# Performance work log

Hardware: AMD Instinct MI355X
Metric: run time of the kernel (lower is better)

The kernel has to match this reference:

```python
import jax, jax.numpy as jnp
import numpy as np

B, T, D, H = 4, 1024, 1024, 16
HD = D // H
EPS = 1e-5


def setup_inputs() -> dict:
    key = jax.random.key(0)
    ks = jax.random.split(key, 8)
    input_tensor = jax.random.normal(ks[0], (B, T, D), dtype=jnp.float32)
    # contiguous valid prefixes (realistic padding mask); True = valid
    lengths = jax.random.randint(ks[1], (B,), T // 2, T + 1)
    sequence_mask = jnp.arange(T)[None, :] < lengths[:, None]
    # online attention mask: causal (True = position allowed)
    attn_mask = jnp.tril(jnp.ones((T, T), dtype=bool))
    scale = 1.0 / np.sqrt(D)
    in_proj_w = jax.random.normal(ks[2], (3 * D, D), dtype=jnp.float32) * scale
    in_proj_b = jnp.zeros((3 * D,), dtype=jnp.float32)
    out_w = jax.random.normal(ks[3], (D, D), dtype=jnp.float32) * scale
    out_b = jnp.zeros((D,), dtype=jnp.float32)
    ln_gamma = jnp.ones((D,), dtype=jnp.float32)
    ln_beta = jnp.zeros((D,), dtype=jnp.float32)
    return {
        "input_tensor": input_tensor,
        "ln_gamma": ln_gamma,
        "ln_beta": ln_beta,
        "in_proj_w": in_proj_w,
        "in_proj_b": in_proj_b,
        "out_w": out_w,
        "out_b": out_b,
        "sequence_mask": sequence_mask,
        "attn_mask": attn_mask,
    }


def reference(input_tensor, ln_gamma, ln_beta, in_proj_w, in_proj_b, out_w, out_b,
              sequence_mask, attn_mask):
    # LayerNorm over last dim
    mu = jnp.mean(input_tensor, axis=-1, keepdims=True)
    var = jnp.mean(jnp.square(input_tensor - mu), axis=-1, keepdims=True)
    x = (input_tensor - mu) * jax.lax.rsqrt(var + EPS) * ln_gamma + ln_beta

    # shared QKV projection (torch MHA packed in_proj)
    qkv = x @ in_proj_w.T + in_proj_b  # [B,T,3D]
    q, k, v = jnp.split(qkv, 3, axis=-1)
    q = q.reshape(B, T, H, HD) * (1.0 / np.sqrt(HD))
    k = k.reshape(B, T, H, HD)
    v = v.reshape(B, T, H, HD)

    scores = jnp.einsum("bqhd,bkhd->bhqk", q, k)  # [B,H,T,T], shared

    keypad = sequence_mask[:, None, None, :]          # True = valid key
    online_ok = keypad & attn_mask[None, None, :, :]  # padding + attn mask
    neg_inf = jnp.float32(-jnp.inf)

    def attend(ok_mask):
        p = jax.nn.softmax(jnp.where(ok_mask, scores, neg_inf), axis=-1)
        o = jnp.einsum("bhqk,bkhd->bqhd", p, v).reshape(B, T, D)
        return o @ out_w.T + out_b

    out_online = attend(online_ok)   # key_padding + attn_mask
    out_offline = attend(keypad)     # key_padding only (full context)
    # training path: cat on dim 0 then view(2, B, T, D)
    return jnp.stack((out_online, out_offline), axis=0)
```

## Files before the change

kernel.cpp:

```cpp
#include <hip/hip_runtime.h>

#define B_ 4
#define T_ 1024
#define D_ 1024
#define H_ 16
#define HD_ 64

typedef unsigned short u16;
typedef __bf16 bf16x8 __attribute__((ext_vector_type(8)));
typedef float f32x4 __attribute__((ext_vector_type(4)));
typedef unsigned short u16x4 __attribute__((ext_vector_type(4)));

__device__ inline u16 f2b(float f) {
    union { float f; unsigned u; } v; v.f = f;
    unsigned r = v.u + 0x7fffu + ((v.u >> 16) & 1u);
    return (u16)(r >> 16);
}

__device__ inline f32x4 mfma16(bf16x8 a, bf16x8 b, f32x4 c) {
    return __builtin_amdgcn_mfma_f32_16x16x32_bf16(a, b, c, 0, 0, 0);
}

__global__ __launch_bounds__(256) void len_kernel(const unsigned char* __restrict__ m,
                                                  int* __restrict__ lens) {
    const int t = threadIdx.x;
    const int b = blockIdx.x;
    const int esz4 = (m[1] == 0);
    int c = 0;
    for (int i = t; i < T_; i += 256) {
        bool v = esz4 ? (((const int*)m)[b * T_ + i] != 0) : (m[b * T_ + i] != 0);
        c += v ? 1 : 0;
    }
#pragma unroll
    for (int off = 1; off < 64; off <<= 1) c += __shfl_xor(c, off);
    __shared__ int red[4];
    if ((t & 63) == 0) red[t >> 6] = c;
    __syncthreads();
    if (t == 0) lens[b] = red[0] + red[1] + red[2] + red[3];
}

__global__ __launch_bounds__(256) void cvt_bf16(const float* __restrict__ in,
                                                u16* __restrict__ out, int n4) {
    int i = blockIdx.x * 256 + threadIdx.x;
    int stride = gridDim.x * 256;
    for (; i < n4; i += stride) {
        float4 v = ((const float4*)in)[i];
        u16x4 o = { f2b(v.x), f2b(v.y), f2b(v.z), f2b(v.w) };
        ((u16x4*)out)[i] = o;
    }
}

__global__ __launch_bounds__(256) void ln_kernel(const float* __restrict__ x,
                                                 const float* __restrict__ g,
                                                 const float* __restrict__ be,
                                                 u16* __restrict__ y) {
    __shared__ float red[8];
    const int row = blockIdx.x;
    const int tid = threadIdx.x;
    const float* xr = x + (size_t)row * D_;
    float4 v = ((const float4*)xr)[tid];
    float s  = v.x + v.y + v.z + v.w;
    float ss = v.x*v.x + v.y*v.y + v.z*v.z + v.w*v.w;
#pragma unroll
    for (int off = 1; off < 64; off <<= 1) {
        s  += __shfl_xor(s, off);
        ss += __shfl_xor(ss, off);
    }
    const int w = tid >> 6;
    if ((tid & 63) == 0) { red[w*2] = s; red[w*2+1] = ss; }
    __syncthreads();
    s  = red[0] + red[2] + red[4] + red[6];
    ss = red[1] + red[3] + red[5] + red[7];
    const float mu = s * (1.f/1024.f);
    const float rs = rsqrtf(ss*(1.f/1024.f) - mu*mu + 1e-5f);
    float4 gv = ((const float4*)g)[tid];
    float4 bv = ((const float4*)be)[tid];
    u16x4 o = { f2b((v.x-mu)*rs*gv.x + bv.x),
                f2b((v.y-mu)*rs*gv.y + bv.y),
                f2b((v.z-mu)*rs*gv.z + bv.z),
                f2b((v.w-mu)*rs*gv.w + bv.w) };
    ((u16x4*)(y + (size_t)row * D_))[tid] = o;
}

template <int EPI>
__global__ __launch_bounds__(512) void gemm_bt(
    const u16* __restrict__ A, const u16* __restrict__ Bw,
    const float* __restrict__ bias, float* __restrict__ Cf,
    u16* __restrict__ Qb, u16* __restrict__ Kb, u16* __restrict__ Vt,
    int M, int N, int K, int MB) {
    __shared__ u16 As[2][256 * 64];
    __shared__ u16 Bs[2][256 * 64];
    const int tid = threadIdx.x;
    const int w = tid >> 6, l = tid & 63;
    const int l15 = l & 15, lg = l >> 4;
    const int wr = w >> 2, wc = w & 3;

    const int nwg = gridDim.x;
    const int q8 = nwg >> 3, r8 = nwg & 7;
    const int xcd = blockIdx.x & 7, pos = blockIdx.x >> 3;
    const int swz = (xcd < r8 ? xcd * (q8 + 1) : r8 * (q8 + 1) + (xcd - r8) * q8) + pos;
    const int m0 = (swz % MB) * 256;
    const int n0 = (swz / MB) * 256;

    const int srow = l >> 3;
    const int scg  = (l & 7) ^ srow;
    const int swa  = l15 & 7;

    f32x4 acc[8][4];
#pragma unroll
    for (int m = 0; m < 8; m++)
#pragma unroll
        for (int n = 0; n < 4; n++) acc[m][n] = (f32x4){0.f, 0.f, 0.f, 0.f};

    const int KS = K >> 6;

    auto stage = [&](int buf, int ks) {
        const int k0 = ks * 64;
#pragma unroll
        for (int it = 0; it < 4; ++it) {
            const int c = w * 4 + it;
            const int row = c * 8 + srow;
            const u16* ga = A  + (size_t)(m0 + row) * K + (k0 + scg * 8);
            const u16* gb = Bw + (size_t)(n0 + row) * K + (k0 + scg * 8);
            __builtin_amdgcn_global_load_lds(
                (const __attribute__((address_space(1))) unsigned int*)ga,
                (__attribute__((address_space(3))) unsigned int*)(&As[buf][c * 512]), 16, 0, 0);
            __builtin_amdgcn_global_load_lds(
                (const __attribute__((address_space(1))) unsigned int*)gb,
                (__attribute__((address_space(3))) unsigned int*)(&Bs[buf][c * 512]), 16, 0, 0);
        }
    };

    stage(0, 0);

    int buf = 0;
    for (int ks = 0; ks < KS; ++ks) {
        if (ks + 1 < KS) {
            stage(buf ^ 1, ks + 1);
            asm volatile("s_waitcnt vmcnt(8)" ::: "memory");
        } else {
            asm volatile("s_waitcnt vmcnt(0)" ::: "memory");
        }
        __builtin_amdgcn_sched_barrier(0);
        __builtin_amdgcn_s_barrier();
        __builtin_amdgcn_sched_barrier(0);
#pragma unroll
        for (int h = 0; h < 2; ++h) {
            bf16x8 bfr[4];
#pragma unroll
            for (int n = 0; n < 4; n++)
                bfr[n] = *(const bf16x8*)&Bs[buf][(wc*64 + n*16 + l15) * 64 + ((h*4 + lg) ^ swa) * 8];
#pragma unroll
            for (int m = 0; m < 8; m++) {
                bf16x8 af = *(const bf16x8*)&As[buf][(wr*128 + m*16 + l15) * 64 + ((h*4 + lg) ^ swa) * 8];
#pragma unroll
                for (int n = 0; n < 4; n++)
                    acc[m][n] = mfma16(af, bfr[n], acc[m][n]);
            }
        }
        __builtin_amdgcn_sched_barrier(0);
        __builtin_amdgcn_s_barrier();
        __builtin_amdgcn_sched_barrier(0);
        buf ^= 1;
    }

#pragma unroll
    for (int m = 0; m < 8; m++) {
#pragma unroll
        for (int n = 0; n < 4; n++) {
            const int col = n0 + wc*64 + n*16 + l15;
            const float bv = bias[col];
            if constexpr (EPI == 0) {
#pragma unroll
                for (int r = 0; r < 4; r++) {
                    const int row = m0 + wr*128 + m*16 + lg*4 + r;
                    Cf[(size_t)row * N + col] = acc[m][n][r] + bv;
                }
            } else {
                const int which = col >> 10;
                const int d = col & 1023;
                const int h = d >> 6, hd = d & 63;
#pragma unroll
                for (int r = 0; r < 4; r++) {
                    const int row = m0 + wr*128 + m*16 + lg*4 + r;
                    const int bb = row >> 10, t = row & 1023;
                    const float v = acc[m][n][r] + bv;
                    const size_t bh = (size_t)bb * H_ + h;
                    if (which == 0)      Qb[(bh * T_ + t) * HD_ + hd] = f2b(v * 0.125f);
                    else if (which == 1) Kb[(bh * T_ + t) * HD_ + hd] = f2b(v);
                    else                 Vt[(bh * HD_ + hd) * T_ + t] = f2b(v);
                }
            }
        }
    }
}

__global__ __launch_bounds__(256) void attn_kernel(
    const u16* __restrict__ Qb, const u16* __restrict__ Kb,
    const u16* __restrict__ Vt, const int* __restrict__ lens,
    u16* __restrict__ Ob) {
    __shared__ u16 Ks[2][64 * 64];
    __shared__ u16 Vs[2][64 * 64];
    __shared__ char Pl[4][2048];
    const int qt  = blockIdx.x;
    const int bh  = blockIdx.y;
    const int b = bh >> 4, h = bh & 15;
    const int tid = threadIdx.x, w = tid >> 6, l = tid & 63;
    const int l15 = l & 15, lg = l >> 4;
    const int len = lens[b];

    const u16* Qh = Qb + (size_t)bh * (T_ * HD_);
    const u16* Kh = Kb + (size_t)bh * (T_ * HD_);
    const u16* Vh = Vt + (size_t)bh * (HD_ * T_);

    const int q0 = qt * 64 + w * 16;
    const int qrow = q0 + l15;

    const bf16x8 qf0 = *(const bf16x8*)(Qh + (size_t)qrow * HD_ + lg * 8);
    const bf16x8 qf1 = *(const bf16x8*)(Qh + (size_t)qrow * HD_ + 32 + lg * 8);

    f32x4 acc0[4], acc1[4];
#pragma unroll
    for (int n = 0; n < 4; n++) {
        acc0[n] = (f32x4){0.f, 0.f, 0.f, 0.f};
        acc1[n] = (f32x4){0.f, 0.f, 0.f, 0.f};
    }
    float l0p = 0.f, l1p = 0.f;

    const int ntk = (len + 63) >> 6;

    char* Pw = &Pl[w][0];
    const int swz = (l15 & 7) << 4;
    const int rsw = l15 & 7;

    const int srow = l >> 3;
    const int scg  = (l & 7) ^ srow;

    const float C1 = 1.44269504f, C0 = -28.8539008f;

    auto stage = [&](int buf, int kt) {
        const int k0 = kt * 64;
#pragma unroll
        for (int c = 0; c < 2; ++c) {
            const int row = (w*2 + c)*8 + srow;
            const u16* gk = Kh + (size_t)(k0 + row) * HD_ + scg*8;
            const u16* gv = Vh + (size_t)row * T_ + k0 + scg*8;
            __builtin_amdgcn_global_load_lds(
                (const __attribute__((address_space(1))) unsigned int*)gk,
                (__attribute__((address_space(3))) unsigned int*)(&Ks[buf][(w*2+c)*512]), 16, 0, 0);
            __builtin_amdgcn_global_load_lds(
                (const __attribute__((address_space(1))) unsigned int*)gv,
                (__attribute__((address_space(3))) unsigned int*)(&Vs[buf][(w*2+c)*512]), 16, 0, 0);
        }
    };

    stage(0, 0);
    __syncthreads();

    int buf = 0;
    for (int kt = 0; kt < ntk; ++kt) {
        if (kt + 1 < ntk) stage(buf ^ 1, kt + 1);
        const int k0 = kt * 64;
        const u16* Kt = &Ks[buf][0];
        const u16* Vl = &Vs[buf][0];

        f32x4 s[4];
#pragma unroll
        for (int n = 0; n < 4; n++) {
            const u16* kr = Kt + (n*16 + l15) * 64;
            bf16x8 kf0 = *(const bf16x8*)&kr[((0 + lg) ^ rsw) * 8];
            bf16x8 kf1 = *(const bf16x8*)&kr[((4 + lg) ^ rsw) * 8];
            f32x4 z = (f32x4){0.f, 0.f, 0.f, 0.f};
            z = mfma16(kf0, qf0, z);
            z = mfma16(kf1, qf1, z);
            s[n] = z;
        }
        bf16x8 vf[4][2];
#pragma unroll
        for (int n = 0; n < 4; n++) {
            const u16* vr = Vl + (n*16 + l15) * 64;
            vf[n][0] = *(const bf16x8*)&vr[((0 + lg) ^ rsw) * 8];
            vf[n][1] = *(const bf16x8*)&vr[((4 + lg) ^ rsw) * 8];
        }
        float pn = 0.f;
#pragma unroll
        for (int n = 0; n < 4; n++) {
            const int kb = k0 + n*16 + lg*4;
#pragma unroll
            for (int r = 0; r < 4; r++) {
                const float e = (kb + r < len) ? exp2f(s[n][r]*C1 + C0) : 0.f;
                s[n][r] = e;
                pn += e;
            }
        }
        const bool diag = (kt == qt);
        if (diag) {
            l0p = l1p;
#pragma unroll
            for (int n = 0; n < 4; n++) acc0[n] = acc1[n];
        }
        l1p += pn;
#pragma unroll
        for (int n = 0; n < 4; n++) {
            u16x4 pk = { f2b(s[n][0]), f2b(s[n][1]), f2b(s[n][2]), f2b(s[n][3]) };
            *(u16x4*)(Pw + ((l15*128 + n*32 + lg*8) ^ swz)) = pk;
        }
#pragma unroll
        for (int kk = 0; kk < 2; ++kk) {
            bf16x8 pa = *(const bf16x8*)(Pw + ((l15*128 + kk*64 + lg*16) ^ swz));
#pragma unroll
            for (int n = 0; n < 4; n++)
                acc1[n] = mfma16(vf[n][kk], pa, acc1[n]);
        }
        if (diag) {
            float pn0 = 0.f;
#pragma unroll
            for (int n = 0; n < 4; n++) {
                const int kb = k0 + n*16 + lg*4;
#pragma unroll
                for (int r = 0; r < 4; r++) {
                    const float e = (kb + r <= qrow) ? s[n][r] : 0.f;
                    s[n][r] = e;
                    pn0 += e;
                }
            }
            l0p += pn0;
#pragma unroll
            for (int n = 0; n < 4; n++) {
                u16x4 pk = { f2b(s[n][0]), f2b(s[n][1]), f2b(s[n][2]), f2b(s[n][3]) };
                *(u16x4*)(Pw + ((l15*128 + n*32 + lg*8) ^ swz)) = pk;
            }
#pragma unroll
            for (int kk = 0; kk < 2; ++kk) {
                bf16x8 pa = *(const bf16x8*)(Pw + ((l15*128 + kk*64 + lg*16) ^ swz));
#pragma unroll
                for (int n = 0; n < 4; n++)
                    acc0[n] = mfma16(vf[n][kk], pa, acc0[n]);
            }
        }
        __syncthreads();
        buf ^= 1;
    }

    if (qt >= ntk) {
        l0p = l1p;
#pragma unroll
        for (int n = 0; n < 4; n++) acc0[n] = acc1[n];
    }

    float l0 = l0p + __shfl_xor(l0p, 16);
    l0 += __shfl_xor(l0, 32);
    float l1 = l1p + __shfl_xor(l1p, 16);
    l1 += __shfl_xor(l1, 32);

    const float inv0 = 1.f / l0;
    const float inv1 = 1.f / l1;
    u16* O0 = Ob + ((size_t)b * T_ + qrow) * D_ + h * HD_;
    u16* O1 = O0 + (size_t)B_ * T_ * D_;
#pragma unroll
    for (int n = 0; n < 4; n++) {
        u16x4 o0 = { f2b(acc0[n][0] * inv0), f2b(acc0[n][1] * inv0),
                     f2b(acc0[n][2] * inv0), f2b(acc0[n][3] * inv0) };
        u16x4 o1 = { f2b(acc1[n][0] * inv1), f2b(acc1[n][1] * inv1),
                     f2b(acc1[n][2] * inv1), f2b(acc1[n][3] * inv1) };
        *(u16x4*)(O0 + n*16 + lg*4) = o0;
        *(u16x4*)(O1 + n*16 + lg*4) = o1;
    }
}

extern "C" void kernel_launch(void* const* d_in, const int* in_sizes, int n_in,
                              void* d_out, int out_size, void* d_ws, size_t ws_size,
                              hipStream_t stream) {
    const float* x_in   = (const float*)d_in[0];
    const float* gamma  = (const float*)d_in[1];
    const float* beta   = (const float*)d_in[2];
    const float* wqkv_f = (const float*)d_in[3];
    const float* bqkv   = (const float*)d_in[4];
    const float* wout_f = (const float*)d_in[5];
    const float* bout   = (const float*)d_in[6];
    const unsigned char* smask = (const unsigned char*)d_in[7];
    float* out = (float*)d_out;

    char* ws = (char*)d_ws;
    u16* xb   = (u16*)(ws);
    u16* wqkv = (u16*)(ws + ((size_t)8  << 20));
    u16* wo   = (u16*)(ws + ((size_t)14 << 20));
    u16* Qb   = (u16*)(ws + ((size_t)16 << 20));
    u16* Kb   = (u16*)(ws + ((size_t)24 << 20));
    u16* Vt   = (u16*)(ws + ((size_t)32 << 20));
    u16* Ob   = (u16*)(ws + ((size_t)40 << 20));
    int* lens = (int*)(ws + ((size_t)56 << 20));

    len_kernel<<<dim3(B_), dim3(256), 0, stream>>>(smask, lens);
    cvt_bf16<<<dim3(1024), dim3(256), 0, stream>>>(wqkv_f, wqkv, (3 * D_ * D_) / 4);
    cvt_bf16<<<dim3(512),  dim3(256), 0, stream>>>(wout_f, wo, (D_ * D_) / 4);
    ln_kernel<<<dim3(B_ * T_), dim3(256), 0, stream>>>(x_in, gamma, beta, xb);
    gemm_bt<1><<<dim3(192), dim3(512), 0, stream>>>(
        xb, wqkv, bqkv, nullptr, Qb, Kb, Vt, B_ * T_, 3 * D_, D_, 16);
    attn_kernel<<<dim3(T_ / 64, B_ * H_), dim3(256), 0, stream>>>(Qb, Kb, Vt, lens, Ob);
    gemm_bt<0><<<dim3(128), dim3(512), 0, stream>>>(
        Ob, wo, bout, out, nullptr, nullptr, nullptr, 2 * B_ * T_, D_, D_, 32);
}
```

Before: 166.5 us.

## Split GEMM k-tile into four phases interleaving prefetch quarters with MFMA

Restructures the GEMM main loop so each 64-wide k-tile runs as four compute phases over quadrants of the output tile. The next tile's global-to-LDS loads are split into four quarters, one issued per phase, instead of all at once. MFMA blocks are wrapped in s_setprio so memory issue and math from different waves can interleave. The intent is to smooth memory traffic and hide load latency, at the cost of more barriers per k-tile, and it depends on the quarter buffers being written only after all waves have finished reading them.

Measured after the change: 173.9 us. 1.04x slower.

```diff
diff --git a/kernel.cpp b/kernel.cpp
--- a/kernel.cpp
+++ b/kernel.cpp
@@ -112,56 +112,84 @@
 #pragma unroll
         for (int n = 0; n < 4; n++) acc[m][n] = (f32x4){0.f, 0.f, 0.f, 0.f};
 
-    const int KS = K >> 6;
-
-    auto stage = [&](int buf, int ks) {
-        const int k0 = ks * 64;
-#pragma unroll
-        for (int it = 0; it < 4; ++it) {
-            const int c = w * 4 + it;
-            const int row = c * 8 + srow;
-            const u16* ga = A  + (size_t)(m0 + row) * K + (k0 + scg * 8);
-            const u16* gb = Bw + (size_t)(n0 + row) * K + (k0 + scg * 8);
+    const int nKt = K >> 6;
+
+    auto stageHalf = [&](int d, int kt, int h) {
+        const int k0 = kt * 64;
+        const u16* src = (h < 2) ? A : Bw;
+        u16* lds = (h < 2) ? &As[d][0] : &Bs[d][0];
+        const int gb = (h < 2) ? m0 : n0;
+        const int rb = (h & 1) * 128 + w * 16;
+#pragma unroll
+        for (int c = 0; c < 2; ++c) {
+            const int row = rb + c * 8;
+            const u16* g = src + (size_t)(gb + row + srow) * K + (k0 + scg * 8);
             __builtin_amdgcn_global_load_lds(
-                (const __attribute__((address_space(1))) unsigned int*)ga,
-                (__attribute__((address_space(3))) unsigned int*)(&As[buf][c * 512]), 16, 0, 0);
-            __builtin_amdgcn_global_load_lds(
-                (const __attribute__((address_space(1))) unsigned int*)gb,
-                (__attribute__((address_space(3))) unsigned int*)(&Bs[buf][c * 512]), 16, 0, 0);
+                (const __attribute__((address_space(1))) unsigned int*)g,
+                (__attribute__((address_space(3))) unsigned int*)(lds + row * 64), 16, 0, 0);
         }
     };
 
-    stage(0, 0);
-
-    int buf = 0;
-    for (int ks = 0; ks < KS; ++ks) {
-        if (ks + 1 < KS) {
-            stage(buf ^ 1, ks + 1);
-            asm volatile("s_waitcnt vmcnt(8)" ::: "memory");
-        } else {
-            asm volatile("s_waitcnt vmcnt(0)" ::: "memory");
-        }
-        __builtin_amdgcn_sched_barrier(0);
-        __builtin_amdgcn_s_barrier();
-        __builtin_amdgcn_sched_barrier(0);
-#pragma unroll
-        for (int h = 0; h < 2; ++h) {
-            bf16x8 bfr[4];
-#pragma unroll
-            for (int n = 0; n < 4; n++)
-                bfr[n] = *(const bf16x8*)&Bs[buf][(wc*64 + n*16 + l15) * 64 + ((h*4 + lg) ^ swa) * 8];
-#pragma unroll
-            for (int m = 0; m < 8; m++) {
-                bf16x8 af = *(const bf16x8*)&As[buf][(wr*128 + m*16 + l15) * 64 + ((h*4 + lg) ^ swa) * 8];
-#pragma unroll
-                for (int n = 0; n < 4; n++)
-                    acc[m][n] = mfma16(af, bfr[n], acc[m][n]);
-            }
-        }
-        __builtin_amdgcn_sched_barrier(0);
-        __builtin_amdgcn_s_barrier();
-        __builtin_amdgcn_sched_barrier(0);
-        buf ^= 1;
+#pragma unroll
+    for (int h = 0; h < 4; ++h) stageHalf(0, 0, h);
+
+    for (int kt = 0; kt < nKt; ++kt) {
+        const int d = kt & 1;
+#pragma unroll
+        for (int ph = 0; ph < 4; ++ph) {
+            const int mh = ph >> 1, nh = ph & 1;
+            bf16x8 af[4][2], bfr[2][2];
+            if (ph == 0) {
+                if (kt + 1 < nKt) {
+                    stageHalf(d ^ 1, kt + 1, 0);
+                    asm volatile("s_waitcnt vmcnt(2)" ::: "memory");
+                } else {
+                    asm volatile("s_waitcnt vmcnt(0)" ::: "memory");
+                }
+                __builtin_amdgcn_sched_barrier(0);
+                __builtin_amdgcn_s_barrier();
+                __builtin_amdgcn_sched_barrier(0);
+#pragma unroll
+                for (int i = 0; i < 4; ++i)
+#pragma unroll
+                    for (int kk = 0; kk < 2; ++kk)
+                        af[i][kk] = *(const bf16x8*)&As[d][(wr*128 + (mh*4+i)*16 + l15) * 64 + ((kk*4 + lg) ^ swa) * 8];
+#pragma unroll
+                for (int j = 0; j < 2; ++j)
+#pragma unroll
+                    for (int kk = 0; kk < 2; ++kk)
+                        bfr[j][kk] = *(const bf16x8*)&Bs[d][(wc*64 + (nh*2+j)*16 + l15) * 64 + ((kk*4 + lg) ^ swa) * 8];
+            } else {
+#pragma unroll
+                for (int i = 0; i < 4; ++i)
+#pragma unroll
+                    for (int kk = 0; kk < 2; ++kk)
+                        af[i][kk] = *(const bf16x8*)&As[d][(wr*128 + (mh*4+i)*16 + l15) * 64 + ((kk*4 + lg) ^ swa) * 8];
+#pragma unroll
+                for (int j = 0; j < 2; ++j)
+#pragma unroll
+                    for (int kk = 0; kk < 2; ++kk)
+                        bfr[j][kk] = *(const bf16x8*)&Bs[d][(wc*64 + (nh*2+j)*16 + l15) * 64 + ((kk*4 + lg) ^ swa) * 8];
+                if (kt + 1 < nKt) stageHalf(d ^ 1, kt + 1, ph);
+                __builtin_amdgcn_sched_barrier(0);
+                __builtin_amdgcn_s_barrier();
+                __builtin_amdgcn_sched_barrier(0);
+            }
+            asm volatile("s_waitcnt lgkmcnt(0)" ::: "memory");
+            __builtin_amdgcn_sched_barrier(0);
+            __builtin_amdgcn_s_setprio(1);
+#pragma unroll
+            for (int kk = 0; kk < 2; ++kk)
+#pragma unroll
+                for (int i = 0; i < 4; ++i)
+#pragma unroll
+                    for (int j = 0; j < 2; ++j)
+                        acc[mh*4+i][nh*2+j] = mfma16(af[i][kk], bfr[j][kk], acc[mh*4+i][nh*2+j]);
+            __builtin_amdgcn_s_setprio(0);
+            __builtin_amdgcn_sched_barrier(0);
+            __builtin_amdgcn_s_barrier();
+            __builtin_amdgcn_sched_barrier(0);
+        }
     }
 
 #pragma unroll
```
